# Kernel optimization log

Measured on AMD Instinct MI355X. Metric: run time of the kernel, lower is better.

## Reference

```python
import jax, jax.numpy as jnp
import numpy as np

N = 16384      # batch size
F = 1024       # n_features
H = 256        # n_dim (latent)


def setup_inputs() -> dict:
    key = jax.random.key(0)
    ks = jax.random.split(key, 6)
    X = jax.random.normal(ks[0], (N, F), dtype=jnp.float32)
    We = jax.random.normal(ks[1], (F, H), dtype=jnp.float32) / np.sqrt(F).astype(np.float32)
    be = jnp.zeros((H,), dtype=jnp.float32)
    Wd = jax.random.normal(ks[2], (H, F), dtype=jnp.float32) / np.sqrt(H).astype(np.float32)
    bd = jnp.zeros((F,), dtype=jnp.float32)
    Wc = jax.random.normal(ks[3], (H, 1), dtype=jnp.float32) / np.sqrt(H).astype(np.float32)
    bc = jnp.zeros((1,), dtype=jnp.float32)
    s = jax.random.randint(ks[4], (N,), 0, 2, dtype=jnp.int32)  # protected attribute labels in {0,1}
    return {"X": X, "We": We, "be": be, "Wd": Wd, "bd": bd, "Wc": Wc, "bc": bc, "s": s, "p": 1}


def reference(X, We, be, Wd, bd, Wc, bc, s, p):
    # encoder / decoder (single Linear each, as in the default NRL construction)
    g = X @ We + be                      # [N, H]
    rec = g @ Wd + bd                    # [N, F]
    mse_mean = jnp.mean((rec - X) ** 2)  # MSELoss is built with reduction='sum' but forward uses torch.mean(pow(...)) directly

    # critic scores for ALL rows (critics share weights: [module]*n_protected)
    c = (g @ Wc + bc)[:, 0]              # [N]

    # masked pairwise L1: sum_{i in P, j notin P} |c_i - c_j|
    mp = (s == p)                        # rows where s == p
    mpf = mp.astype(c.dtype)
    mrf = (~mp).astype(c.dtype)
    Dmat = jnp.abs(c[:, None] - c[None, :])   # [N, N] pairwise L1 (cdist equivalent)
    total = mpf @ (Dmat @ mrf)                # mp^T D mr == cdist(c_p, c_rest, p=1).sum()

    w_dist_count = mp.sum()                   # == w_dist.shape[0] (number of protected rows)
    w_dist_mean = total / w_dist_count.astype(c.dtype)

    return (mse_mean, jnp.asarray(rec.shape[0]), w_dist_mean, w_dist_count)
```

## Files before the change

### kernel.cpp

```cpp
#include <hip/hip_runtime.h>
#include <hip/hip_bf16.h>
#include <cstdint>

#define NR 16384
#define NF 1024
#define NH 256

typedef __bf16 bf16x8 __attribute__((ext_vector_type(8)));
typedef float f32x4 __attribute__((ext_vector_type(4)));
typedef unsigned short us8 __attribute__((ext_vector_type(8)));

static __device__ __forceinline__ unsigned short f2bf(float f) {
    unsigned u = __float_as_uint(f);
    u += 0x7FFFu + ((u >> 16) & 1u);
    return (unsigned short)(u >> 16);
}


__global__ __launch_bounds__(256) void prep_kernel(
    const float* __restrict__ We, const float* __restrict__ Wd,
    unsigned short* __restrict__ Wepk, unsigned short* __restrict__ Wdpk,
    float* __restrict__ hdr) {
    const int b = blockIdx.x, t = threadIdx.x;
    if (b == 0 && t < 192) hdr[t] = 0.f;
    if (b < 128) {
        const int k0 = b, c = t;
        const int kc = k0 >> 2, q = k0 & 3, nb = c >> 4, li = c & 15;
        us8 v;
#pragma unroll
        for (int e = 0; e < 8; e++)
            v[e] = f2bf(We[(size_t)(k0 * 8 + e) * NH + c]);
        *(us8*)&Wepk[((size_t)(nb * 32 + kc)) * 512 + (q * 16 + li) * 8] = v;
    } else {
        const int idx = b - 128;
        const int k0 = idx >> 2, c = (idx & 3) * 256 + t;
        const int kc = k0 >> 2, q = k0 & 3, nb = c >> 4, li = c & 15;
        us8 v;
#pragma unroll
        for (int e = 0; e < 8; e++)
            v[e] = f2bf(Wd[(size_t)(k0 * 8 + e) * NF + c]);
        *(us8*)&Wdpk[((size_t)(nb * 8 + kc)) * 512 + (q * 16 + li) * 8] = v;
    }
}

__global__ __launch_bounds__(256) void fused_kernel(
    const float* __restrict__ X,
    const unsigned short* __restrict__ Wepk, const unsigned short* __restrict__ Wdpk,
    const float* __restrict__ be, const float* __restrict__ bd,
    const float* __restrict__ Wc, const int* __restrict__ s, const int* __restrict__ pv,
    float* __restrict__ cP, float* __restrict__ cR, float* __restrict__ hdr) {
    __shared__ union {
        unsigned short xa[16 * 1024];
        struct {
            unsigned short gs[16 * 256];
            float credu[4][16];
            float msred[4];
        } p2;
    } u;
    const int t = threadIdx.x;
    const int b = blockIdx.x, m0 = b * 16;
    const int w = t >> 6, lane = t & 63, q = lane >> 4, li = lane & 15;
    const int wn = w * 64;

    {
#pragma unroll
        for (int rr = 0; rr < 4; ++rr) {
            const int r = w * 4 + rr;
            const float* xrow = X + (size_t)(m0 + r) * NF;
#pragma unroll
            for (int p = 0; p < 2; ++p) {
                float4 lo = *(const float4*)(xrow + p * 512 + lane * 8);
                float4 hi = *(const float4*)(xrow + p * 512 + lane * 8 + 4);
                us8 v;
                v[0] = f2bf(lo.x); v[1] = f2bf(lo.y); v[2] = f2bf(lo.z); v[3] = f2bf(lo.w);
                v[4] = f2bf(hi.x); v[5] = f2bf(hi.y); v[6] = f2bf(hi.z); v[7] = f2bf(hi.w);
                const int ch = p * 64 + lane;
                *(us8*)&u.xa[r * 1024 + ((ch ^ r) & 127) * 8] = v;
            }
        }
    }
    __syncthreads();

    const unsigned short* Bp[4];
#pragma unroll
    for (int j = 0; j < 4; j++)
        Bp[j] = Wepk + ((size_t)(w * 4 + j) * 32) * 512 + lane * 8;

    us8 fb[4][4];
#pragma unroll
    for (int z = 0; z < 4; ++z)
#pragma unroll
        for (int j = 0; j < 4; j++) fb[z][j] = *(const us8*)(Bp[j] + z * 512);

    f32x4 acc[4] = {};
#pragma unroll
    for (int kc = 0; kc < 32; ++kc) {
        const int cb = kc & 3;
        const int chl = kc * 4 + q;
        const int ph0 = (chl ^ li) & 127;
        bf16x8 a0 = __builtin_bit_cast(bf16x8, *(const us8*)&u.xa[li * 1024 + ph0 * 8]);
#pragma unroll
        for (int j = 0; j < 4; j++) {
            bf16x8 bf = __builtin_bit_cast(bf16x8, fb[cb][j]);
            acc[j] = __builtin_amdgcn_mfma_f32_16x16x32_bf16(bf, a0, acc[j], 0, 0, 0);
        }
        if (kc + 4 < 32) {
#pragma unroll
            for (int j = 0; j < 4; j++) fb[cb][j] = *(const us8*)(Bp[j] + (kc + 4) * 512);
        }
    }
    __syncthreads();

    const unsigned short* Wp = Wdpk + lane * 8;
    us8 gb[4][4];
#pragma unroll
    for (int z = 0; z < 4; ++z)
#pragma unroll
        for (int j = 0; j < 4; j++)
            gb[z][j] = *(const us8*)(Wp + ((size_t)((w * 4 + j) * 8 + z)) * 512);

    {
        float csum = 0.f;
        const int ml = li;
#pragma unroll
        for (int j = 0; j < 4; j++) {
            const int colb = wn + j * 16 + q * 4;
            float4 be4 = *(const float4*)&be[colb];
            float4 wc4 = *(const float4*)&Wc[colb];
            float v0 = acc[j][0] + be4.x;
            float v1 = acc[j][1] + be4.y;
            float v2 = acc[j][2] + be4.z;
            float v3 = acc[j][3] + be4.w;
            csum += v0 * wc4.x + v1 * wc4.y + v2 * wc4.z + v3 * wc4.w;
            ushort4 st = { f2bf(v0), f2bf(v1), f2bf(v2), f2bf(v3) };
            const int phys = (colb >> 3) ^ ml;
            *(ushort4*)&u.p2.gs[ml * 256 + phys * 8 + (q & 1) * 4] = st;
        }
        csum += __shfl_down(csum, 32);
        csum += __shfl_down(csum, 16);
        if (lane < 16) u.p2.credu[w][lane] = csum;
    }
    __syncthreads();

    if (t < 16) {
        float cs = u.p2.credu[0][t] + u.p2.credu[1][t] +
                   u.p2.credu[2][t] + u.p2.credu[3][t];
        bool pr = (s[m0 + t] == pv[0]);
        unsigned long long mk = __ballot(pr);
        int np = __popcll(mk);
        int baseP = 0, baseR = 0;
        if (t == 0) {
            baseP = atomicAdd((int*)hdr + 129, np);
            baseR = atomicAdd((int*)hdr + 130, 16 - np);
        }
        baseP = __shfl(baseP, 0);
        baseR = __shfl(baseR, 0);
        int offP = __popcll(mk & ((1ull << t) - 1ull));
        int offR = t - offP;
        if (pr) cP[baseP + offP] = cs; else cR[baseR + offR] = cs;
    }

    float lsum = 0.f;
    f32x4 a2[4] = {};
#pragma unroll
    for (int it = 0; it < 32; ++it) {
        const int cb = it & 3, pass = it >> 3, kc = it & 7;
        const int ml = li;
        const int phys = (kc * 4 + q) ^ ml;
        bf16x8 af = __builtin_bit_cast(bf16x8, *(const us8*)&u.p2.gs[ml * 256 + phys * 8]);
#pragma unroll
        for (int j = 0; j < 4; j++) {
            bf16x8 bf = __builtin_bit_cast(bf16x8, gb[cb][j]);
            a2[j] = __builtin_amdgcn_mfma_f32_16x16x32_bf16(bf, af, a2[j], 0, 0, 0);
        }
        if (it + 4 < 32) {
            const int p2i = (it + 4) >> 3, k2 = (it + 4) & 7;
#pragma unroll
            for (int j = 0; j < 4; j++)
                gb[cb][j] = *(const us8*)(Wp + ((size_t)((p2i * 16 + w * 4 + j) * 8 + k2)) * 512);
        }
        if (kc == 7) {
            const size_t rowoff = (size_t)(m0 + li) * NF;
#pragma unroll
            for (int j = 0; j < 4; j++) {
                const int colb = pass * 256 + wn + j * 16 + q * 4;
                float4 bd4 = *(const float4*)&bd[colb];
                float4 xr  = *(const float4*)&X[rowoff + colb];
                float d0 = a2[j][0] + bd4.x - xr.x;
                float d1 = a2[j][1] + bd4.y - xr.y;
                float d2 = a2[j][2] + bd4.z - xr.z;
                float d3 = a2[j][3] + bd4.w - xr.w;
                lsum += d0 * d0 + d1 * d1 + d2 * d2 + d3 * d3;
                a2[j] = (f32x4){0.f, 0.f, 0.f, 0.f};
            }
        }
    }
#pragma unroll
    for (int o = 32; o; o >>= 1) lsum += __shfl_down(lsum, o);
    if (lane == 0) u.p2.msred[w] = lsum;
    __syncthreads();
    if (t == 0)
        atomicAdd(&hdr[b & 63], u.p2.msred[0] + u.p2.msred[1] +
                                u.p2.msred[2] + u.p2.msred[3]);
}

__global__ __launch_bounds__(256) void pair_fin_kernel(
    const float* __restrict__ cP, const float* __restrict__ cR,
    float* __restrict__ hdr, float* __restrict__ out) {
    __shared__ float sj[1024];
    __shared__ float red[256];
    __shared__ int win;
    const int nP = ((const int*)hdr)[129];
    const int nR = ((const int*)hdr)[130];
    const int jb = blockIdx.x * 1024;
    int jn = nR - jb; if (jn < 0) jn = 0; if (jn > 1024) jn = 1024;
    float sum = 0.f;
    if (jn > 0 && blockIdx.y * 512 < nP) {
        for (int j = threadIdx.x; j < 1024; j += 256)
            sj[j] = (jb + j < nR) ? cR[jb + j] : 0.f;
        __syncthreads();
        const int a0 = blockIdx.y * 512 + threadIdx.x, a1 = a0 + 256;
        const float ca0 = (a0 < nP) ? cP[a0] : 0.f;
        const float ca1 = (a1 < nP) ? cP[a1] : 0.f;
        float s0 = 0.f, s1 = 0.f;
#pragma unroll 8
        for (int j4 = 0; j4 < 256; j4++) {
            float4 v = *(const float4*)&sj[j4 * 4];
            s0 += fabsf(ca0 - v.x) + fabsf(ca0 - v.y) + fabsf(ca0 - v.z) + fabsf(ca0 - v.w);
            s1 += fabsf(ca1 - v.x) + fabsf(ca1 - v.y) + fabsf(ca1 - v.z) + fabsf(ca1 - v.w);
        }
        float pad = (float)(1024 - jn);
        s0 -= pad * fabsf(ca0);
        s1 -= pad * fabsf(ca1);
        if (a0 >= nP) s0 = 0.f;
        if (a1 >= nP) s1 = 0.f;
        sum = s0 + s1;
#pragma unroll
        for (int o = 32; o; o >>= 1) sum += __shfl_down(sum, o);
        if ((threadIdx.x & 63) == 0 && sum != 0.f)
            atomicAdd(&hdr[64 + ((blockIdx.y * 16 + blockIdx.x) & 63)], sum);
    }
    __threadfence();
    __syncthreads();
    if (threadIdx.x == 0)
        win = (atomicAdd((int*)(hdr + 128), 1) == 16 * 32 - 1) ? 1 : 0;
    __syncthreads();
    if (win) {
        float v = (threadIdx.x < 128) ? atomicAdd(&hdr[threadIdx.x], 0.f) : 0.f;
        red[threadIdx.x] = v;
        __syncthreads();
        if (threadIdx.x == 0) {
            float ms = 0.f, ps = 0.f;
            for (int i = 0; i < 64; i++) { ms += red[i]; ps += red[64 + i]; }
            int np = atomicAdd((int*)(hdr + 129), 0);
            out[0] = ms / (float)((size_t)NR * NF);
            out[1] = (float)NR;
            out[2] = ps / (float)np;
            out[3] = (float)np;
        }
    }
}

extern "C" void kernel_launch(void* const* d_in, const int* in_sizes, int n_in,
                              void* d_out, int out_size, void* d_ws, size_t ws_size,
                              hipStream_t stream) {
    const float* X  = (const float*)d_in[0];
    const float* We = (const float*)d_in[1];
    const float* be = (const float*)d_in[2];
    const float* Wd = (const float*)d_in[3];
    const float* bd = (const float*)d_in[4];
    const float* Wc = (const float*)d_in[5];
    const int*   s  = (const int*)d_in[7];
    const int*   pv = (const int*)d_in[8];

    char* ws = (char*)d_ws;
    float* hdr = (float*)ws;
    float* cP  = (float*)(ws + 1024);
    float* cR  = (float*)(ws + 1024 + 65536);
    unsigned short* Wepk = (unsigned short*)(ws + 1024 + 2 * 65536);
    unsigned short* Wdpk = Wepk + (size_t)NH * NF;

    prep_kernel<<<256, 256, 0, stream>>>(We, Wd, Wepk, Wdpk, hdr);
    fused_kernel<<<1024, 256, 0, stream>>>(X, Wepk, Wdpk, be, bd, Wc, s, pv, cP, cR, hdr);
    pair_fin_kernel<<<dim3(16, 32), 256, 0, stream>>>(cP, cR, hdr, (float*)d_out);
}
```

Measured before the change: 208.8 us.

## Widen fused block to 64 rows with 8 waves and K-chunked X staging

The fused encoder/decoder kernel now handles 64 rows per block with 512 threads instead of 16 rows with 256, so each weight fragment loaded from global memory feeds four MFMA row tiles. X is staged into shared memory in four 256-column chunks, and the next chunk is prefetched into registers while MFMAs run on the current one. This cuts weight traffic per row. In exchange the grid drops to 256 blocks, which may underfill the GPU, and the larger accumulator arrays raise register pressure.

New measurement: 182.7 us. 12.5% less time.

```diff
diff --git a/kernel.cpp b/kernel.cpp
--- a/kernel.cpp
+++ b/kernel.cpp
@@ -43,115 +43,134 @@
     }
 }
 
-__global__ __launch_bounds__(256) void fused_kernel(
+__global__ __launch_bounds__(512) void fused_kernel(
     const float* __restrict__ X,
     const unsigned short* __restrict__ Wepk, const unsigned short* __restrict__ Wdpk,
     const float* __restrict__ be, const float* __restrict__ bd,
     const float* __restrict__ Wc, const int* __restrict__ s, const int* __restrict__ pv,
     float* __restrict__ cP, float* __restrict__ cR, float* __restrict__ hdr) {
     __shared__ union {
-        unsigned short xa[16 * 1024];
+        unsigned short xa[64 * 256];
         struct {
-            unsigned short gs[16 * 256];
-            float credu[4][16];
-            float msred[4];
+            unsigned short gs[64 * 256];
+            float credu[8][64];
+            float msred[8];
         } p2;
     } u;
     const int t = threadIdx.x;
-    const int b = blockIdx.x, m0 = b * 16;
+    const int b = blockIdx.x, m0 = b * 64;
     const int w = t >> 6, lane = t & 63, q = lane >> 4, li = lane & 15;
-    const int wn = w * 64;
+
+    const int srow = w * 8;
+    const int sch = lane >> 1, shalf = lane & 1;
 
     {
 #pragma unroll
-        for (int rr = 0; rr < 4; ++rr) {
-            const int r = w * 4 + rr;
-            const float* xrow = X + (size_t)(m0 + r) * NF;
-#pragma unroll
-            for (int p = 0; p < 2; ++p) {
-                float4 lo = *(const float4*)(xrow + p * 512 + lane * 8);
-                float4 hi = *(const float4*)(xrow + p * 512 + lane * 8 + 4);
-                us8 v;
-                v[0] = f2bf(lo.x); v[1] = f2bf(lo.y); v[2] = f2bf(lo.z); v[3] = f2bf(lo.w);
-                v[4] = f2bf(hi.x); v[5] = f2bf(hi.y); v[6] = f2bf(hi.z); v[7] = f2bf(hi.w);
-                const int ch = p * 64 + lane;
-                *(us8*)&u.xa[r * 1024 + ((ch ^ r) & 127) * 8] = v;
-            }
-        }
-    }
-    __syncthreads();
-
-    const unsigned short* Bp[4];
-#pragma unroll
-    for (int j = 0; j < 4; j++)
-        Bp[j] = Wepk + ((size_t)(w * 4 + j) * 32) * 512 + lane * 8;
-
-    us8 fb[4][4];
-#pragma unroll
-    for (int z = 0; z < 4; ++z)
-#pragma unroll
-        for (int j = 0; j < 4; j++) fb[z][j] = *(const us8*)(Bp[j] + z * 512);
-
-    f32x4 acc[4] = {};
-#pragma unroll
-    for (int kc = 0; kc < 32; ++kc) {
-        const int cb = kc & 3;
-        const int chl = kc * 4 + q;
-        const int ph0 = (chl ^ li) & 127;
-        bf16x8 a0 = __builtin_bit_cast(bf16x8, *(const us8*)&u.xa[li * 1024 + ph0 * 8]);
-#pragma unroll
-        for (int j = 0; j < 4; j++) {
-            bf16x8 bf = __builtin_bit_cast(bf16x8, fb[cb][j]);
-            acc[j] = __builtin_amdgcn_mfma_f32_16x16x32_bf16(bf, a0, acc[j], 0, 0, 0);
-        }
-        if (kc + 4 < 32) {
-#pragma unroll
-            for (int j = 0; j < 4; j++) fb[cb][j] = *(const us8*)(Bp[j] + (kc + 4) * 512);
-        }
-    }
-    __syncthreads();
-
-    const unsigned short* Wp = Wdpk + lane * 8;
-    us8 gb[4][4];
-#pragma unroll
-    for (int z = 0; z < 4; ++z)
-#pragma unroll
-        for (int j = 0; j < 4; j++)
-            gb[z][j] = *(const us8*)(Wp + ((size_t)((w * 4 + j) * 8 + z)) * 512);
-
-    {
+        for (int rr = 0; rr < 8; ++rr) {
+            const int r = srow + rr;
+            float4 v4 = *(const float4*)(X + (size_t)(m0 + r) * NF + lane * 4);
+            ushort4 st = { f2bf(v4.x), f2bf(v4.y), f2bf(v4.z), f2bf(v4.w) };
+            const int phys = (sch ^ (r & 31)) & 31;
+            *(ushort4*)&u.xa[r * 256 + phys * 8 + shalf * 4] = st;
+        }
+    }
+    __syncthreads();
+
+    const unsigned short* Bp[2];
+#pragma unroll
+    for (int j = 0; j < 2; j++)
+        Bp[j] = Wepk + ((size_t)(w * 2 + j) * 32) * 512 + lane * 8;
+
+    us8 fb[8][2];
+#pragma unroll
+    for (int z = 0; z < 8; ++z)
+#pragma unroll
+        for (int j = 0; j < 2; j++) fb[z][j] = *(const us8*)(Bp[j] + z * 512);
+
+    f32x4 acc[4][2] = {};
+    float4 xn[8];
+
+#pragma unroll
+    for (int ks = 0; ks < 4; ++ks) {
+        if (ks < 3) {
+#pragma unroll
+            for (int rr = 0; rr < 8; ++rr)
+                xn[rr] = *(const float4*)(X + (size_t)(m0 + srow + rr) * NF +
+                                          (ks + 1) * 256 + lane * 4);
+        }
+#pragma unroll
+        for (int kcl = 0; kcl < 8; ++kcl) {
+            const int kcg = ks * 8 + kcl;
+            const int cb = kcg & 7;
+            bf16x8 a[4];
+#pragma unroll
+            for (int mi = 0; mi < 4; ++mi) {
+                const int r = mi * 16 + li;
+                const int phys = ((kcl * 4 + q) ^ (r & 31)) & 31;
+                a[mi] = __builtin_bit_cast(bf16x8, *(const us8*)&u.xa[r * 256 + phys * 8]);
+            }
+#pragma unroll
+            for (int j = 0; j < 2; ++j) {
+                bf16x8 bf = __builtin_bit_cast(bf16x8, fb[cb][j]);
+#pragma unroll
+                for (int mi = 0; mi < 4; ++mi)
+                    acc[mi][j] = __builtin_amdgcn_mfma_f32_16x16x32_bf16(bf, a[mi], acc[mi][j], 0, 0, 0);
+            }
+            if (kcg + 8 < 32) {
+#pragma unroll
+                for (int j = 0; j < 2; j++) fb[cb][j] = *(const us8*)(Bp[j] + (kcg + 8) * 512);
+            }
+        }
+        __syncthreads();
+        if (ks < 3) {
+#pragma unroll
+            for (int rr = 0; rr < 8; ++rr) {
+                const int r = srow + rr;
+                ushort4 st = { f2bf(xn[rr].x), f2bf(xn[rr].y),
+                               f2bf(xn[rr].z), f2bf(xn[rr].w) };
+                const int phys = (sch ^ (r & 31)) & 31;
+                *(ushort4*)&u.xa[r * 256 + phys * 8 + shalf * 4] = st;
+            }
+            __syncthreads();
+        }
+    }
+
+#pragma unroll
+    for (int mi = 0; mi < 4; ++mi) {
         float csum = 0.f;
-        const int ml = li;
-#pragma unroll
-        for (int j = 0; j < 4; j++) {
-            const int colb = wn + j * 16 + q * 4;
+        const int ml = mi * 16 + li;
+#pragma unroll
+        for (int j = 0; j < 2; ++j) {
+            const int colb = w * 32 + j * 16 + q * 4;
             float4 be4 = *(const float4*)&be[colb];
             float4 wc4 = *(const float4*)&Wc[colb];
-            float v0 = acc[j][0] + be4.x;
-            float v1 = acc[j][1] + be4.y;
-            float v2 = acc[j][2] + be4.z;
-            float v3 = acc[j][3] + be4.w;
+            float v0 = acc[mi][j][0] + be4.x;
+            float v1 = acc[mi][j][1] + be4.y;
+            float v2 = acc[mi][j][2] + be4.z;
+            float v3 = acc[mi][j][3] + be4.w;
             csum += v0 * wc4.x + v1 * wc4.y + v2 * wc4.z + v3 * wc4.w;
             ushort4 st = { f2bf(v0), f2bf(v1), f2bf(v2), f2bf(v3) };
-            const int phys = (colb >> 3) ^ ml;
+            const int ch = colb >> 3;
+            const int phys = (ch ^ (ml & 31)) & 31;
             *(ushort4*)&u.p2.gs[ml * 256 + phys * 8 + (q & 1) * 4] = st;
         }
         csum += __shfl_down(csum, 32);
         csum += __shfl_down(csum, 16);
-        if (lane < 16) u.p2.credu[w][lane] = csum;
-    }
-    __syncthreads();
-
-    if (t < 16) {
-        float cs = u.p2.credu[0][t] + u.p2.credu[1][t] +
-                   u.p2.credu[2][t] + u.p2.credu[3][t];
+        if (lane < 16) u.p2.credu[w][mi * 16 + lane] = csum;
+    }
+    __syncthreads();
+
+    if (t < 64) {
+        float cs = 0.f;
+#pragma unroll
+        for (int ww = 0; ww < 8; ++ww) cs += u.p2.credu[ww][t];
         bool pr = (s[m0 + t] == pv[0]);
         unsigned long long mk = __ballot(pr);
         int np = __popcll(mk);
         int baseP = 0, baseR = 0;
         if (t == 0) {
             baseP = atomicAdd((int*)hdr + 129, np);
-            baseR = atomicAdd((int*)hdr + 130, 16 - np);
+            baseR = atomicAdd((int*)hdr + 130, 64 - np);
         }
         baseP = __shfl(baseP, 0);
         baseR = __shfl(baseR, 0);
@@ -161,37 +180,53 @@
     }
 
     float lsum = 0.f;
-    f32x4 a2[4] = {};
-#pragma unroll
-    for (int it = 0; it < 32; ++it) {
-        const int cb = it & 3, pass = it >> 3, kc = it & 7;
-        const int ml = li;
-        const int phys = (kc * 4 + q) ^ ml;
-        bf16x8 af = __builtin_bit_cast(bf16x8, *(const us8*)&u.p2.gs[ml * 256 + phys * 8]);
-#pragma unroll
-        for (int j = 0; j < 4; j++) {
-            bf16x8 bf = __builtin_bit_cast(bf16x8, gb[cb][j]);
-            a2[j] = __builtin_amdgcn_mfma_f32_16x16x32_bf16(bf, af, a2[j], 0, 0, 0);
-        }
-        if (it + 4 < 32) {
-            const int p2i = (it + 4) >> 3, k2 = (it + 4) & 7;
-#pragma unroll
-            for (int j = 0; j < 4; j++)
-                gb[cb][j] = *(const us8*)(Wp + ((size_t)((p2i * 16 + w * 4 + j) * 8 + k2)) * 512);
-        }
-        if (kc == 7) {
-            const size_t rowoff = (size_t)(m0 + li) * NF;
-#pragma unroll
-            for (int j = 0; j < 4; j++) {
-                const int colb = pass * 256 + wn + j * 16 + q * 4;
+    const unsigned short* Wp = Wdpk + lane * 8;
+#pragma unroll
+    for (int pass = 0; pass < 2; ++pass) {
+        const int nb0 = pass * 32 + w * 4;
+        us8 gb[4][4];
+#pragma unroll
+        for (int z = 0; z < 4; ++z)
+#pragma unroll
+            for (int j = 0; j < 4; ++j)
+                gb[z][j] = *(const us8*)(Wp + ((size_t)((nb0 + j) * 8 + z)) * 512);
+        f32x4 a2[4][4] = {};
+#pragma unroll
+        for (int kc = 0; kc < 8; ++kc) {
+            const int cb = kc & 3;
+            bf16x8 af[4];
+#pragma unroll
+            for (int mi = 0; mi < 4; ++mi) {
+                const int ml = mi * 16 + li;
+                const int phys = ((kc * 4 + q) ^ (ml & 31)) & 31;
+                af[mi] = __builtin_bit_cast(bf16x8, *(const us8*)&u.p2.gs[ml * 256 + phys * 8]);
+            }
+#pragma unroll
+            for (int j = 0; j < 4; ++j) {
+                bf16x8 bf = __builtin_bit_cast(bf16x8, gb[cb][j]);
+#pragma unroll
+                for (int mi = 0; mi < 4; ++mi)
+                    a2[mi][j] = __builtin_amdgcn_mfma_f32_16x16x32_bf16(bf, af[mi], a2[mi][j], 0, 0, 0);
+            }
+            if (kc + 4 < 8) {
+#pragma unroll
+                for (int j = 0; j < 4; ++j)
+                    gb[cb][j] = *(const us8*)(Wp + ((size_t)((nb0 + j) * 8 + kc + 4)) * 512);
+            }
+        }
+#pragma unroll
+        for (int mi = 0; mi < 4; ++mi) {
+            const size_t rowoff = (size_t)(m0 + mi * 16 + li) * NF;
+#pragma unroll
+            for (int j = 0; j < 4; ++j) {
+                const int colb = pass * 512 + w * 64 + j * 16 + q * 4;
                 float4 bd4 = *(const float4*)&bd[colb];
                 float4 xr  = *(const float4*)&X[rowoff + colb];
-                float d0 = a2[j][0] + bd4.x - xr.x;
-                float d1 = a2[j][1] + bd4.y - xr.y;
-                float d2 = a2[j][2] + bd4.z - xr.z;
-                float d3 = a2[j][3] + bd4.w - xr.w;
+                float d0 = a2[mi][j][0] + bd4.x - xr.x;
+                float d1 = a2[mi][j][1] + bd4.y - xr.y;
+                float d2 = a2[mi][j][2] + bd4.z - xr.z;
+                float d3 = a2[mi][j][3] + bd4.w - xr.w;
                 lsum += d0 * d0 + d1 * d1 + d2 * d2 + d3 * d3;
-                a2[j] = (f32x4){0.f, 0.f, 0.f, 0.f};
             }
         }
     }
@@ -199,9 +234,12 @@
     for (int o = 32; o; o >>= 1) lsum += __shfl_down(lsum, o);
     if (lane == 0) u.p2.msred[w] = lsum;
     __syncthreads();
-    if (t == 0)
-        atomicAdd(&hdr[b & 63], u.p2.msred[0] + u.p2.msred[1] +
-                                u.p2.msred[2] + u.p2.msred[3]);
+    if (t == 0) {
+        float ms = 0.f;
+#pragma unroll
+        for (int ww = 0; ww < 8; ++ww) ms += u.p2.msred[ww];
+        atomicAdd(&hdr[b & 63], ms);
+    }
 }
 
 __global__ __launch_bounds__(256) void pair_fin_kernel(
@@ -281,6 +319,6 @@
     unsigned short* Wdpk = Wepk + (size_t)NH * NF;
 
     prep_kernel<<<256, 256, 0, stream>>>(We, Wd, Wepk, Wdpk, hdr);
-    fused_kernel<<<1024, 256, 0, stream>>>(X, Wepk, Wdpk, be, bd, Wc, s, pv, cP, cR, hdr);
+    fused_kernel<<<256, 512, 0, stream>>>(X, Wepk, Wdpk, be, bd, Wc, s, pv, cP, cR, hdr);
     pair_fin_kernel<<<dim3(16, 32), 256, 0, stream>>>(cP, cR, hdr, (float*)d_out);
 }
```
